# Performance work log

Hardware: AMD Instinct MI355X
Metric: run time of the kernel (lower is better)

## Reference

```python
import jax, jax.numpy as jnp
import numpy as np

B = 4096
UNITS = 1024
OUT_STEPS = 128
W_SCALE = 0.02  # keep gates out of hard saturation


def setup_inputs() -> dict:
    key = jax.random.key(0)
    k1, k2, k3, k4 = jax.random.split(key, 4)
    features = jax.random.normal(k1, (B, UNITS // 2), dtype=jnp.float32)
    kernel = jax.random.normal(k2, (1, 4 * UNITS), dtype=jnp.float32) * W_SCALE
    recurrent_kernel = jax.random.normal(k3, (UNITS, 4 * UNITS), dtype=jnp.float32) * W_SCALE
    bias = jnp.zeros((4 * UNITS,), dtype=jnp.float32)
    dense_w = jax.random.normal(k4, (UNITS, 1), dtype=jnp.float32) * W_SCALE
    dense_b = jnp.zeros((1,), dtype=jnp.float32)
    return {
        "features": features,
        "kernel": kernel,
        "recurrent_kernel": recurrent_kernel,
        "bias": bias,
        "dense_w": dense_w,
        "dense_b": dense_b,
    }


def reference(features, kernel, recurrent_kernel, bias, dense_w, dense_b):
    # State init: h = c = concat([features, features], axis=1) -> [B, UNITS]
    h0 = jnp.concatenate([features, features], axis=1)
    c0 = h0
    x0 = jnp.zeros((features.shape[0], 1), dtype=features.dtype)

    def step(carry, _):
        x, h, c = carry
        # Keras LSTMCell: gates ordered (i, f, g, o)
        z = x @ kernel + h @ recurrent_kernel + bias  # [B, 4*UNITS]
        zi, zf, zg, zo = jnp.split(z, 4, axis=1)
        i = jax.nn.sigmoid(zi)
        f = jax.nn.sigmoid(zf)
        g = jnp.tanh(zg)
        o = jax.nn.sigmoid(zo)
        c_new = f * c + i * g
        h_new = o * jnp.tanh(c_new)
        pred = h_new @ dense_w + dense_b  # [B, 1], fed back as next input
        return (pred, h_new, c_new), pred

    _, preds = jax.lax.scan(step, (x0, h0, c0), None, length=OUT_STEPS)
    # preds: [T, B, 1] -> [B, T, 1] (matches tf.stack + transpose [1,0,2])
    return jnp.transpose(preds, (1, 0, 2))
```

## Files before the change

### kernel.cpp

```cpp
#include <hip/hip_runtime.h>
#include <hip/hip_bf16.h>
#include <stdint.h>

#define BATCH 4096
#define UNITS 1024
#define NSTEP 128

typedef __attribute__((ext_vector_type(4))) float f32x4;
typedef __attribute__((ext_vector_type(8))) short s16x8;

__device__ __forceinline__ void gload16(const void* g, void* l) {
  __builtin_amdgcn_global_load_lds(
      (const __attribute__((address_space(1))) unsigned int*)g,
      (__attribute__((address_space(3))) unsigned int*)l, 16, 0, 0);
}

__device__ __forceinline__ void block_barrier() {
  asm volatile("" ::: "memory");
  __builtin_amdgcn_s_barrier();
  asm volatile("" ::: "memory");
}

__device__ __forceinline__ float fsigmoid(float x) {
  return 1.0f / (1.0f + __expf(-x));
}
__device__ __forceinline__ float ftanh(float x) {
  return 1.0f - 2.0f / (__expf(2.0f * x) + 1.0f);
}

__global__ void prep_weights(const float* __restrict__ R,
                             const float* __restrict__ ker,
                             const float* __restrict__ dw,
                             __hip_bfloat16* __restrict__ Rt0,
                             __hip_bfloat16* __restrict__ Rt1) {
  __shared__ float tile[32][33];
  __shared__ float dws[32];
  const int n0 = blockIdx.x * 32;
  const int k0 = blockIdx.y * 32;
  const int tx = threadIdx.x;
  const int ty = threadIdx.y;
#pragma unroll
  for (int i = 0; i < 4; ++i) {
    int k = ty + i * 8;
    tile[k][tx] = R[(size_t)(k0 + k) * 4096 + n0 + tx];
  }
  if (ty == 0) dws[tx] = dw[k0 + tx];
  __syncthreads();
#pragma unroll
  for (int i = 0; i < 4; ++i) {
    int n = ty + i * 8;
    float v = tile[tx][n];
    int gn = n0 + n, gk = k0 + tx;
    int g = gn >> 10, u = gn & 1023;
    int q = u >> 6, wc = (u >> 4) & 3, ul = u & 15;
    int np = q * 256 + (g >> 1) * 128 + wc * 32 + (g & 1) * 16 + ul;
    size_t o = (size_t)np * 1024 + gk;
    Rt0[o] = __float2bfloat16(v);
    Rt1[o] = __float2bfloat16(v + dws[tx] * ker[gn]);
  }
}

__global__ void prep_state(const float* __restrict__ feat,
                           const float* __restrict__ bias,
                           const float* __restrict__ ker,
                           const float* __restrict__ db,
                           float* __restrict__ bias1,
                           __hip_bfloat16* __restrict__ hA,
                           float* __restrict__ c,
                           float* __restrict__ out) {
  const int total = BATCH * UNITS;
  const float dbv = db[0];
  for (int i = blockIdx.x * blockDim.x + threadIdx.x; i < total;
       i += gridDim.x * blockDim.x) {
    int b = i >> 10, u = i & 1023;
    float v = feat[b * 512 + (u & 511)];
    hA[i] = __float2bfloat16(v);
    c[i] = v;
    if (i < 4096) bias1[i] = bias[i] + dbv * ker[i];
    if (i < BATCH * NSTEP) out[i] = dbv;
  }
}

__global__ __launch_bounds__(512, 2) void lstm_step(
    const __hip_bfloat16* __restrict__ hin,
    const __hip_bfloat16* __restrict__ Bp,
    const float* __restrict__ biasv,
    float* __restrict__ c,
    __hip_bfloat16* __restrict__ hout,
    const float* __restrict__ dw,
    float* __restrict__ out, int t) {
  extern __shared__ char lds[];
  const int tid = threadIdx.x;
  const int lane = tid & 63;
  const int w = tid >> 6;
  const int l15 = lane & 15;
  const int lhi = lane >> 4;
  const int wr = w >> 2;
  const int wc = w & 3;

  const int bi = blockIdx.x;
  const int xcd = bi & 7, slot = bi >> 3;
  const int bx = (xcd & 3) * 4 + (slot & 3);
  const int by = (xcd >> 2) * 8 + (slot >> 2);

  const int ucol = by * 64 + wc * 16 + l15;
  const float dwv = dw[ucol];

  f32x4 acc[8][4];
#pragma unroll
  for (int g = 0; g < 4; ++g) {
    float bg = biasv[g * 1024 + ucol];
#pragma unroll
    for (int m = 0; m < 8; ++m) acc[m][g] = (f32x4){bg, bg, bg, bg};
  }

  const char* Asrc = (const char*)(hin + (size_t)bx * 256 * 1024);
  const char* Bsrc = (const char*)(Bp + (size_t)by * 256 * 1024);
  const int swz = (l15 & 7) << 4;

  auto STAGE = [&](const char* src, int rowoff, int kt, char* dstbase) {
#pragma unroll
    for (int i = 0; i < 2; ++i) {
      int chunk = i * 512 + tid;
      int row = chunk >> 3, s = chunk & 7;
      gload16(src + (size_t)(rowoff + row) * 2048 + kt * 128 +
                  ((s * 16) ^ ((row & 7) << 4)),
              dstbase + i * 8192 + w * 1024 + lane * 16);
    }
  };

  STAGE(Asrc, 0,   0, lds);
  STAGE(Bsrc, 0,   0, lds + 32768);
  STAGE(Bsrc, 128, 0, lds + 32768 + 16384);
  STAGE(Asrc, 128, 0, lds + 16384);

  for (int kt = 0; kt < 16; ++kt) {
    const char* Ab = lds + (kt & 1) * 65536;
    const char* Bb = Ab + 32768;
    char* Sd = lds + ((kt + 1) & 1) * 65536;
    const bool pf = (kt < 15);

    s16x8 al[4][2], bl[2][2], bh[2][2], ah[4][2];

    asm volatile("s_waitcnt vmcnt(4)" ::: "memory");
    block_barrier();
#pragma unroll
    for (int m = 0; m < 4; ++m) {
      int row = wr * 64 + m * 16 + l15;
#pragma unroll
      for (int kk = 0; kk < 2; ++kk)
        al[m][kk] = *(const s16x8*)(Ab + row * 128 + ((kk * 64 + lhi * 16) ^ swz));
    }
#pragma unroll
    for (int g = 0; g < 2; ++g) {
      int row = wc * 32 + g * 16 + l15;
#pragma unroll
      for (int kk = 0; kk < 2; ++kk)
        bl[g][kk] = *(const s16x8*)(Bb + row * 128 + ((kk * 64 + lhi * 16) ^ swz));
    }
    if (pf) STAGE(Asrc, 0, kt + 1, Sd);
    asm volatile("s_waitcnt lgkmcnt(0)" ::: "memory");
    __builtin_amdgcn_sched_barrier(0);
    __builtin_amdgcn_s_setprio(1);
#pragma unroll
    for (int m = 0; m < 4; ++m)
#pragma unroll
      for (int g = 0; g < 2; ++g)
#pragma unroll
        for (int kk = 0; kk < 2; ++kk)
          acc[m][g] = __builtin_amdgcn_mfma_f32_16x16x32_bf16(
              al[m][kk], bl[g][kk], acc[m][g], 0, 0, 0);
    __builtin_amdgcn_s_setprio(0);

    if (pf) asm volatile("s_waitcnt vmcnt(4)" ::: "memory");
    else    asm volatile("s_waitcnt vmcnt(2)" ::: "memory");
    block_barrier();
#pragma unroll
    for (int g = 0; g < 2; ++g) {
      int row = 128 + wc * 32 + g * 16 + l15;
#pragma unroll
      for (int kk = 0; kk < 2; ++kk)
        bh[g][kk] = *(const s16x8*)(Bb + row * 128 + ((kk * 64 + lhi * 16) ^ swz));
    }
    if (pf) STAGE(Bsrc, 0, kt + 1, Sd + 32768);
    asm volatile("s_waitcnt lgkmcnt(0)" ::: "memory");
    __builtin_amdgcn_sched_barrier(0);
    __builtin_amdgcn_s_setprio(1);
#pragma unroll
    for (int m = 0; m < 4; ++m)
#pragma unroll
      for (int g = 0; g < 2; ++g)
#pragma unroll
        for (int kk = 0; kk < 2; ++kk)
          acc[m][g + 2] = __builtin_amdgcn_mfma_f32_16x16x32_bf16(
              al[m][kk], bh[g][kk], acc[m][g + 2], 0, 0, 0);
    __builtin_amdgcn_s_setprio(0);

    if (pf) asm volatile("s_waitcnt vmcnt(4)" ::: "memory");
    else    asm volatile("s_waitcnt vmcnt(0)" ::: "memory");
    block_barrier();
#pragma unroll
    for (int m = 0; m < 4; ++m) {
      int row = 128 + wr * 64 + m * 16 + l15;
#pragma unroll
      for (int kk = 0; kk < 2; ++kk)
        ah[m][kk] = *(const s16x8*)(Ab + row * 128 + ((kk * 64 + lhi * 16) ^ swz));
    }
    if (pf) STAGE(Bsrc, 128, kt + 1, Sd + 32768 + 16384);
    asm volatile("s_waitcnt lgkmcnt(0)" ::: "memory");
    __builtin_amdgcn_sched_barrier(0);
    __builtin_amdgcn_s_setprio(1);
#pragma unroll
    for (int m = 0; m < 4; ++m)
#pragma unroll
      for (int g = 0; g < 2; ++g)
#pragma unroll
        for (int kk = 0; kk < 2; ++kk)
          acc[m + 4][g + 2] = __builtin_amdgcn_mfma_f32_16x16x32_bf16(
              ah[m][kk], bh[g][kk], acc[m + 4][g + 2], 0, 0, 0);
    __builtin_amdgcn_s_setprio(0);

    if (pf) STAGE(Asrc, 128, kt + 1, Sd + 16384);
    __builtin_amdgcn_s_setprio(1);
#pragma unroll
    for (int m = 0; m < 4; ++m)
#pragma unroll
      for (int g = 0; g < 2; ++g)
#pragma unroll
        for (int kk = 0; kk < 2; ++kk)
          acc[m + 4][g] = __builtin_amdgcn_mfma_f32_16x16x32_bf16(
              ah[m][kk], bl[g][kk], acc[m + 4][g], 0, 0, 0);
    __builtin_amdgcn_s_setprio(0);
  }

#pragma unroll
  for (int m = 0; m < 8; ++m) {
#pragma unroll
    for (int j = 0; j < 4; ++j) {
      int b = bx * 256 + (m >> 2) * 128 + wr * 64 + (m & 3) * 16 + lhi * 4 + j;
      size_t ci = (size_t)b * 1024 + ucol;
      float zi = acc[m][0][j], zf = acc[m][1][j];
      float zg = acc[m][2][j], zo = acc[m][3][j];
      float ig = fsigmoid(zi), fg = fsigmoid(zf);
      float gg = ftanh(zg), og = fsigmoid(zo);
      float cn = fg * c[ci] + ig * gg;
      c[ci] = cn;
      float hn = og * ftanh(cn);
      hout[ci] = __float2bfloat16(hn);
      float p = hn * dwv;
      p += __shfl_xor(p, 1);
      p += __shfl_xor(p, 2);
      p += __shfl_xor(p, 4);
      p += __shfl_xor(p, 8);
      if (l15 == 0) atomicAdd(&out[(size_t)b * NSTEP + t], p);
    }
  }
}

extern "C" void kernel_launch(void* const* d_in, const int* in_sizes, int n_in,
                              void* d_out, int out_size, void* d_ws, size_t ws_size,
                              hipStream_t stream) {
  const float* feat = (const float*)d_in[0];
  const float* ker  = (const float*)d_in[1];
  const float* R    = (const float*)d_in[2];
  const float* bias = (const float*)d_in[3];
  const float* dw   = (const float*)d_in[4];
  const float* db   = (const float*)d_in[5];
  float* out = (float*)d_out;

  char* ws = (char*)d_ws;
  const size_t MB = 1024 * 1024;
  __hip_bfloat16* Rt0 = (__hip_bfloat16*)(ws);
  __hip_bfloat16* Rt1 = (__hip_bfloat16*)(ws + 8 * MB);
  float* bias1 = (float*)(ws + 16 * MB);
  __hip_bfloat16* hA = (__hip_bfloat16*)(ws + 16 * MB + 65536);
  __hip_bfloat16* hB = (__hip_bfloat16*)(ws + 24 * MB + 65536);
  float* cbuf = (float*)(ws + 32 * MB + 65536);

  hipFuncSetAttribute((const void*)lstm_step,
                      hipFuncAttributeMaxDynamicSharedMemorySize, 131072);

  prep_weights<<<dim3(128, 32), dim3(32, 8), 0, stream>>>(R, ker, dw, Rt0, Rt1);
  prep_state<<<4096, 256, 0, stream>>>(feat, bias, ker, db, bias1, hA, cbuf, out);

  for (int t = 0; t < NSTEP; ++t) {
    const __hip_bfloat16* hin = (t & 1) ? hB : hA;
    __hip_bfloat16* hout = (t & 1) ? hA : hB;
    lstm_step<<<256, 512, 131072, stream>>>(
        hin, (t == 0) ? Rt0 : Rt1, (t == 0) ? bias : bias1, cbuf, hout, dw, out, t);
  }
}
```

Before: 6.112 ms.

## Software-pipeline LDS fragment reads across k-tiles with double-buffered B fragments

Restructures the k-loop of the recurrent GEMM step so that the A-low and B-low fragments for the next tile are read from LDS during the current tile's MFMA phases. Global-to-LDS prefetch now runs up to two tiles ahead, and partial lgkmcnt waits replace full drains. The aim is to hide LDS read latency behind MFMA work and reduce barrier stalls. In exchange it uses more registers for the extra fragment buffers and relies on tricky hand-written vmcnt/lgkmcnt counts that could race if any are wrong.

```diff
diff --git a/kernel.cpp b/kernel.cpp
--- a/kernel.cpp
+++ b/kernel.cpp
@@ -27,6 +27,19 @@
 __device__ __forceinline__ float ftanh(float x) {
   return 1.0f - 2.0f / (__expf(2.0f * x) + 1.0f);
 }
+
+#define MMA(Afr, Bfr, MO, GO)                                              \
+  do {                                                                     \
+    __builtin_amdgcn_s_setprio(1);                                         \
+    _Pragma("unroll") for (int m_ = 0; m_ < 4; ++m_)                       \
+    _Pragma("unroll") for (int g_ = 0; g_ < 2; ++g_)                       \
+    _Pragma("unroll") for (int k_ = 0; k_ < 2; ++k_)                       \
+        acc[(MO) + m_][(GO) + g_] =                                        \
+            __builtin_amdgcn_mfma_f32_16x16x32_bf16(                       \
+                Afr[m_][k_], Bfr[g_][k_], acc[(MO) + m_][(GO) + g_],       \
+                0, 0, 0);                                                  \
+    __builtin_amdgcn_s_setprio(0);                                         \
+  } while (0)
 
 __global__ void prep_weights(const float* __restrict__ R,
                              const float* __restrict__ ker,
@@ -113,6 +126,7 @@
 #pragma unroll
     for (int m = 0; m < 8; ++m) acc[m][g] = (f32x4){bg, bg, bg, bg};
   }
+  asm volatile("" :: "v"(dwv));
 
   const char* Asrc = (const char*)(hin + (size_t)bx * 256 * 1024);
   const char* Bsrc = (const char*)(Bp + (size_t)by * 256 * 1024);
@@ -129,108 +143,109 @@
     }
   };
 
+  s16x8 al[4][2], ah[4][2], bh[2][2], blA[2][2], blB[2][2];
+
+  auto RD_AL = [&](const char* Ab, s16x8 (&d)[4][2]) {
+#pragma unroll
+    for (int m = 0; m < 4; ++m) {
+      int row = wr * 64 + m * 16 + l15;
+#pragma unroll
+      for (int kk = 0; kk < 2; ++kk)
+        d[m][kk] = *(const s16x8*)(Ab + row * 128 + ((kk * 64 + lhi * 16) ^ swz));
+    }
+  };
+  auto RD_AH = [&](const char* Ab, s16x8 (&d)[4][2]) {
+#pragma unroll
+    for (int m = 0; m < 4; ++m) {
+      int row = 128 + wr * 64 + m * 16 + l15;
+#pragma unroll
+      for (int kk = 0; kk < 2; ++kk)
+        d[m][kk] = *(const s16x8*)(Ab + row * 128 + ((kk * 64 + lhi * 16) ^ swz));
+    }
+  };
+  auto RD_BL = [&](const char* Bb, s16x8 (&d)[2][2]) {
+#pragma unroll
+    for (int g = 0; g < 2; ++g) {
+      int row = wc * 32 + g * 16 + l15;
+#pragma unroll
+      for (int kk = 0; kk < 2; ++kk)
+        d[g][kk] = *(const s16x8*)(Bb + row * 128 + ((kk * 64 + lhi * 16) ^ swz));
+    }
+  };
+  auto RD_BH = [&](const char* Bb, s16x8 (&d)[2][2]) {
+#pragma unroll
+    for (int g = 0; g < 2; ++g) {
+      int row = 128 + wc * 32 + g * 16 + l15;
+#pragma unroll
+      for (int kk = 0; kk < 2; ++kk)
+        d[g][kk] = *(const s16x8*)(Bb + row * 128 + ((kk * 64 + lhi * 16) ^ swz));
+    }
+  };
+
   STAGE(Asrc, 0,   0, lds);
   STAGE(Bsrc, 0,   0, lds + 32768);
   STAGE(Bsrc, 128, 0, lds + 32768 + 16384);
   STAGE(Asrc, 128, 0, lds + 16384);
-
-  for (int kt = 0; kt < 16; ++kt) {
-    const char* Ab = lds + (kt & 1) * 65536;
+  STAGE(Asrc, 0,   1, lds + 65536);
+  STAGE(Bsrc, 0,   1, lds + 65536 + 32768);
+  asm volatile("s_waitcnt vmcnt(4)" ::: "memory");
+  block_barrier();
+  RD_AL(lds, al);
+  RD_BL(lds + 32768, blA);
+
+  auto TILE = [&](int kt, s16x8 (&blCur)[2][2], s16x8 (&blNext)[2][2]) {
+    const int p = kt & 1, q = p ^ 1;
+    const char* Ab = lds + p * 65536;
     const char* Bb = Ab + 32768;
-    char* Sd = lds + ((kt + 1) & 1) * 65536;
-    const bool pf = (kt < 15);
-
-    s16x8 al[4][2], bl[2][2], bh[2][2], ah[4][2];
-
+    char* SdN = lds + q * 65536;
+    char* SdP = lds + p * 65536;
+
+    RD_BH(Bb, bh);
+    if (kt < 15) STAGE(Bsrc, 128, kt + 1, SdN + 32768 + 16384);
+    asm volatile("s_waitcnt lgkmcnt(4)" ::: "memory");
+    __builtin_amdgcn_sched_barrier(0);
+    MMA(al, blCur, 0, 0);
+    if (kt == 15) asm volatile("s_waitcnt vmcnt(0)" ::: "memory");
+    else          asm volatile("s_waitcnt vmcnt(4)" ::: "memory");
+    block_barrier();
+
+    RD_AH(Ab, ah);
+    if (kt < 15) STAGE(Asrc, 128, kt + 1, SdN + 16384);
+    asm volatile("s_waitcnt lgkmcnt(8)" ::: "memory");
+    __builtin_amdgcn_sched_barrier(0);
+    MMA(al, bh, 0, 2);
     asm volatile("s_waitcnt vmcnt(4)" ::: "memory");
     block_barrier();
-#pragma unroll
-    for (int m = 0; m < 4; ++m) {
-      int row = wr * 64 + m * 16 + l15;
-#pragma unroll
-      for (int kk = 0; kk < 2; ++kk)
-        al[m][kk] = *(const s16x8*)(Ab + row * 128 + ((kk * 64 + lhi * 16) ^ swz));
-    }
-#pragma unroll
-    for (int g = 0; g < 2; ++g) {
-      int row = wc * 32 + g * 16 + l15;
-#pragma unroll
-      for (int kk = 0; kk < 2; ++kk)
-        bl[g][kk] = *(const s16x8*)(Bb + row * 128 + ((kk * 64 + lhi * 16) ^ swz));
-    }
-    if (pf) STAGE(Asrc, 0, kt + 1, Sd);
-    asm volatile("s_waitcnt lgkmcnt(0)" ::: "memory");
+
+    if (kt < 15) {
+      RD_AL(SdN, al);
+      if (kt < 14) STAGE(Asrc, 0, kt + 2, SdP);
+      asm volatile("s_waitcnt lgkmcnt(8)" ::: "memory");
+    } else {
+      asm volatile("s_waitcnt lgkmcnt(0)" ::: "memory");
+    }
     __builtin_amdgcn_sched_barrier(0);
-    __builtin_amdgcn_s_setprio(1);
-#pragma unroll
-    for (int m = 0; m < 4; ++m)
-#pragma unroll
-      for (int g = 0; g < 2; ++g)
-#pragma unroll
-        for (int kk = 0; kk < 2; ++kk)
-          acc[m][g] = __builtin_amdgcn_mfma_f32_16x16x32_bf16(
-              al[m][kk], bl[g][kk], acc[m][g], 0, 0, 0);
-    __builtin_amdgcn_s_setprio(0);
-
-    if (pf) asm volatile("s_waitcnt vmcnt(4)" ::: "memory");
-    else    asm volatile("s_waitcnt vmcnt(2)" ::: "memory");
+    MMA(ah, bh, 4, 2);
+    asm volatile("s_waitcnt vmcnt(4)" ::: "memory");
     block_barrier();
-#pragma unroll
-    for (int g = 0; g < 2; ++g) {
-      int row = 128 + wc * 32 + g * 16 + l15;
-#pragma unroll
-      for (int kk = 0; kk < 2; ++kk)
-        bh[g][kk] = *(const s16x8*)(Bb + row * 128 + ((kk * 64 + lhi * 16) ^ swz));
-    }
-    if (pf) STAGE(Bsrc, 0, kt + 1, Sd + 32768);
-    asm volatile("s_waitcnt lgkmcnt(0)" ::: "memory");
+
+    if (kt < 15) {
+      RD_BL(SdN + 32768, blNext);
+      if (kt < 14) STAGE(Bsrc, 0, kt + 2, SdP + 32768);
+      asm volatile("s_waitcnt lgkmcnt(4)" ::: "memory");
+    } else {
+      asm volatile("s_waitcnt lgkmcnt(0)" ::: "memory");
+    }
     __builtin_amdgcn_sched_barrier(0);
-    __builtin_amdgcn_s_setprio(1);
-#pragma unroll
-    for (int m = 0; m < 4; ++m)
-#pragma unroll
-      for (int g = 0; g < 2; ++g)
-#pragma unroll
-        for (int kk = 0; kk < 2; ++kk)
-          acc[m][g + 2] = __builtin_amdgcn_mfma_f32_16x16x32_bf16(
-              al[m][kk], bh[g][kk], acc[m][g + 2], 0, 0, 0);
-    __builtin_amdgcn_s_setprio(0);
-
-    if (pf) asm volatile("s_waitcnt vmcnt(4)" ::: "memory");
-    else    asm volatile("s_waitcnt vmcnt(0)" ::: "memory");
+    MMA(ah, blCur, 4, 0);
+    if (kt == 14) asm volatile("s_waitcnt vmcnt(2)" ::: "memory");
+    else          asm volatile("s_waitcnt vmcnt(4)" ::: "memory");
     block_barrier();
-#pragma unroll
-    for (int m = 0; m < 4; ++m) {
-      int row = 128 + wr * 64 + m * 16 + l15;
-#pragma unroll
-      for (int kk = 0; kk < 2; ++kk)
-        ah[m][kk] = *(const s16x8*)(Ab + row * 128 + ((kk * 64 + lhi * 16) ^ swz));
-    }
-    if (pf) STAGE(Bsrc, 128, kt + 1, Sd + 32768 + 16384);
-    asm volatile("s_waitcnt lgkmcnt(0)" ::: "memory");
-    __builtin_amdgcn_sched_barrier(0);
-    __builtin_amdgcn_s_setprio(1);
-#pragma unroll
-    for (int m = 0; m < 4; ++m)
-#pragma unroll
-      for (int g = 0; g < 2; ++g)
-#pragma unroll
-        for (int kk = 0; kk < 2; ++kk)
-          acc[m + 4][g + 2] = __builtin_amdgcn_mfma_f32_16x16x32_bf16(
-              ah[m][kk], bh[g][kk], acc[m + 4][g + 2], 0, 0, 0);
-    __builtin_amdgcn_s_setprio(0);
-
-    if (pf) STAGE(Asrc, 128, kt + 1, Sd + 16384);
-    __builtin_amdgcn_s_setprio(1);
-#pragma unroll
-    for (int m = 0; m < 4; ++m)
-#pragma unroll
-      for (int g = 0; g < 2; ++g)
-#pragma unroll
-        for (int kk = 0; kk < 2; ++kk)
-          acc[m + 4][g] = __builtin_amdgcn_mfma_f32_16x16x32_bf16(
-              ah[m][kk], bl[g][kk], acc[m + 4][g], 0, 0, 0);
-    __builtin_amdgcn_s_setprio(0);
+  };
+
+  for (int k2 = 0; k2 < 16; k2 += 2) {
+    TILE(k2,     blA, blB);
+    TILE(k2 + 1, blB, blA);
   }
 
 #pragma unroll
```

After: 17.25 ms. 182% more time.
